# Performance work log

Measured on AMD Instinct MI355X. Metric: run time of the kernel, lower is better.

Reference implementation:

```python
import jax, jax.numpy as jnp
import numpy as np

EPS_POS = 1e-6  # eps passed explicitly for positive cosine_similarity
EPS_NEG = 1e-8  # torch default eps for negative cosine_similarity


def setup_inputs() -> dict:
    key = jax.random.key(0)
    dvectors = jax.random.normal(key, (1024, 32, 256), dtype=jnp.float32)
    w = jnp.array([10.0], dtype=jnp.float32)
    b = jnp.array([-5.0], dtype=jnp.float32)
    return {"dvectors": dvectors, "w": w, "b": b}


def reference(dvectors, w, b):
    S, U, D = dvectors.shape

    # ---- positive: leave-one-out centroid within each speaker ----
    # pos_centroid[s,u] = mean of speaker s's utterances excluding u
    pos_cent = (dvectors.sum(axis=1, keepdims=True) - dvectors) / (U - 1)  # [S,U,D]
    dn_pos = dvectors / jnp.maximum(
        jnp.linalg.norm(dvectors, axis=-1, keepdims=True), EPS_POS)
    cn_pos = pos_cent / jnp.maximum(
        jnp.linalg.norm(pos_cent, axis=-1, keepdims=True), EPS_POS)
    pos_cos = jnp.sum(dn_pos * cn_pos, axis=-1)  # [S,U]

    # ---- negative: full (non-LOO) centroids of every speaker ----
    cent = dvectors.mean(axis=1)  # [S,D]
    dn = dvectors / jnp.maximum(
        jnp.linalg.norm(dvectors, axis=-1, keepdims=True), EPS_NEG)
    cn = cent / jnp.maximum(jnp.linalg.norm(cent, axis=-1, keepdims=True), EPS_NEG)
    all_cos = jnp.einsum('sud,td->sut', dn, cn)  # [S,U,S] cos(dvec[s,u], cent[t])

    # own-speaker entries all_cos[s,u,s] are EXCLUDED from neg_sim
    own = jnp.take_along_axis(
        all_cos, jnp.arange(S, dtype=jnp.int32)[:, None, None], axis=2
    ).squeeze(2)  # [S,U]

    pos_mean = jnp.mean(pos_cos)
    neg_mean = (jnp.sum(all_cos) - jnp.sum(own)) / (S * U * (S - 1))

    # scaled sims: w * cos + b  (torch.clamp(self.w, 1e-6) in forward is a no-op)
    w0 = w[0]
    b0 = b[0]
    pos_scaled = w0 * pos_cos + b0  # [S,U]
    neg_scaled = w0 * all_cos + b0  # [S,U,S]

    # logsumexp over the S-1 other speakers (mask own speaker to -inf)
    own_mask = jnp.eye(S, dtype=bool)[:, None, :]  # [S,1,S]
    neg_masked = jnp.where(own_mask, -jnp.inf, neg_scaled)
    lse = jax.nn.logsumexp(neg_masked, axis=2)  # [S,U]

    loss = jnp.mean(-pos_scaled + lse)
    return (loss, pos_mean, neg_mean)
```

## Files before the change

kernel.cpp:

```cpp
#include <hip/hip_runtime.h>
#include <math.h>

#define NS 1024
#define NU 32
#define ND 256
#define NROWS (NS * NU)
#define BM 128
#define NBLK (NROWS / BM)

static constexpr float EPS_POS = 1e-6f;
static constexpr float EPS_NEG = 1e-8f;

typedef __attribute__((ext_vector_type(8))) short bf16x8;
typedef __attribute__((ext_vector_type(4))) float f32x4;

#if __has_builtin(__builtin_amdgcn_exp2f)
#define EXP2F(x) __builtin_amdgcn_exp2f(x)
#else
#define EXP2F(x) exp2f(x)
#endif

static __device__ __forceinline__ unsigned short f2bf(float f) {
    union { float f; unsigned u; } v; v.f = f;
    unsigned r = v.u + 0x7fffu + ((v.u >> 16) & 1u);
    return (unsigned short)(r >> 16);
}

__global__ __launch_bounds__(256) void ge2e_k1(
    const float* __restrict__ dv, unsigned short* __restrict__ cnb,
    float* __restrict__ invn, float* __restrict__ blk_pos)
{
    const int s = blockIdx.x;
    const int tid = threadIdx.x;
    const int wave = tid >> 6;
    const int lane = tid & 63;

    __shared__ float v[NU][ND];
    __shared__ float cs[ND];
    __shared__ float red[16];

    const float* base = dv + (size_t)s * (NU * ND);
    for (int idx = tid; idx < NU * ND; idx += 256) {
        v[idx >> 8][idx & 255] = base[idx];
    }
    __syncthreads();

    {
        float a = 0.f;
        #pragma unroll
        for (int u = 0; u < NU; ++u) a += v[u][tid];
        cs[tid] = a;
    }
    __syncthreads();

    float c = cs[tid] * (1.0f / NU);
    float p = c * c;
    #pragma unroll
    for (int off = 32; off > 0; off >>= 1) p += __shfl_xor(p, off, 64);
    if (lane == 0) red[wave] = p;
    __syncthreads();
    if (tid == 0) red[8] = red[0] + red[1] + red[2] + red[3];
    __syncthreads();
    {
        float rn = 1.0f / fmaxf(sqrtf(red[8]), EPS_NEG);
        cnb[(size_t)s * ND + tid] = f2bf(c * rn);
    }

    const float inv31 = 1.0f / (NU - 1);
    float pos_part = 0.f;
    const float4 cc = *(const float4*)&cs[lane * 4];
    for (int uu = 0; uu < 8; ++uu) {
        const int u = wave * 8 + uu;
        const float4 vv = *(const float4*)&v[u][lane * 4];
        float pv = 0.f, pp = 0.f, px = 0.f;
        float pc;
        pc = (cc.x - vv.x) * inv31; pv += vv.x * vv.x; pp += pc * pc; px += vv.x * pc;
        pc = (cc.y - vv.y) * inv31; pv += vv.y * vv.y; pp += pc * pc; px += vv.y * pc;
        pc = (cc.z - vv.z) * inv31; pv += vv.z * vv.z; pp += pc * pc; px += vv.z * pc;
        pc = (cc.w - vv.w) * inv31; pv += vv.w * vv.w; pp += pc * pc; px += vv.w * pc;
        #pragma unroll
        for (int off = 32; off > 0; off >>= 1) {
            pv += __shfl_xor(pv, off, 64);
            pp += __shfl_xor(pp, off, 64);
            px += __shfl_xor(px, off, 64);
        }
        if (lane == 0) {
            float nv = sqrtf(pv), npc = sqrtf(pp);
            pos_part += px / (fmaxf(nv, EPS_POS) * fmaxf(npc, EPS_POS));
            invn[s * NU + u] = 1.0f / fmaxf(nv, EPS_NEG);
        }
    }
    if (lane == 0) red[4 + wave] = pos_part;
    __syncthreads();
    if (tid == 0) blk_pos[s] = red[4] + red[5] + red[6] + red[7];
}

__global__ __launch_bounds__(512, 2) void ge2e_k2(
    const float* __restrict__ dv, const unsigned short* __restrict__ cnb,
    const float* __restrict__ invn, const float* __restrict__ wp,
    const float* __restrict__ bp, float* __restrict__ blk_neg,
    float* __restrict__ blk_lse)
{
    const int blk = blockIdx.x;
    const int r0 = blk * BM;
    const int tid = threadIdx.x;
    const int w  = tid >> 6;
    const int l  = tid & 63;
    const int lr = l & 15;
    const int lg = l >> 4;
    const int mg = w >> 2;
    const int ng = w & 3;
    const int rsw = lr & 7;

    __shared__ unsigned short Al[BM][264];
    __shared__ unsigned short Bst[2][64][256];
    __shared__ float sinv[BM];
    __shared__ float pse[4][BM];
    __shared__ float psm[4][BM];
    __shared__ float redn[2], redl[2];

    const float w0 = wp[0];
    const float b0 = bp[0];
    const float c2 = w0 * 1.4426950408889634f;

    if (tid < BM) sinv[tid] = invn[r0 + tid];

    unsigned srcb[4], ldso[4];
    #pragma unroll
    for (int i = 0; i < 4; ++i) {
        const int gi = w * 256 + i * 64 + l;
        const int rr = gi >> 5;
        const int gc = gi & 31;
        srcb[i] = (unsigned)(rr * 512 + (gc ^ (rr & 7)) * 16);
        ldso[i] = (unsigned)(w * 256 + i * 64) * 16;
    }
    const char* cnbc = (const char*)cnb;

    #pragma unroll
    for (int i = 0; i < 4; ++i) {
        __builtin_amdgcn_global_load_lds(
            (const __attribute__((address_space(1))) void*)(cnbc + srcb[i]),
            (__attribute__((address_space(3))) void*)((char*)&Bst[0][0][0] + ldso[i]),
            16, 0, 0);
    }
    __syncthreads();

    #pragma unroll
    for (int it = 0; it < 8; ++it) {
        const int i = tid + it * 512;
        const int row = i >> 5, g = i & 31;
        const float* src = dv + (size_t)(r0 + row) * ND + g * 8;
        const float4 x = *(const float4*)src;
        const float4 y = *(const float4*)(src + 4);
        const float sc = sinv[row];
        uint4 pk;
        pk.x = (unsigned)f2bf(x.x * sc) | ((unsigned)f2bf(x.y * sc) << 16);
        pk.y = (unsigned)f2bf(x.z * sc) | ((unsigned)f2bf(x.w * sc) << 16);
        pk.z = (unsigned)f2bf(y.x * sc) | ((unsigned)f2bf(y.y * sc) << 16);
        pk.w = (unsigned)f2bf(y.z * sc) | ((unsigned)f2bf(y.w * sc) << 16);
        *(uint4*)&Al[row][g * 8] = pk;
    }
    __syncthreads();

    bf16x8 afr[4][8];
    #pragma unroll
    for (int mt = 0; mt < 4; ++mt)
        #pragma unroll
        for (int kt = 0; kt < 8; ++kt)
            afr[mt][kt] = *(const bf16x8*)&Al[mg * 64 + mt * 16 + lr][kt * 32 + lg * 8];
    #pragma unroll
    for (int mt = 0; mt < 4; ++mt)
        #pragma unroll
        for (int kt = 0; kt < 8; ++kt)
            asm volatile("" : "+v"(afr[mt][kt]));

    float se[4][4], sm[4][4];
    #pragma unroll
    for (int mt = 0; mt < 4; ++mt)
        #pragma unroll
        for (int r = 0; r < 4; ++r) { se[mt][r] = 0.f; sm[mt][r] = 0.f; }

    int town[4];
    #pragma unroll
    for (int mt = 0; mt < 4; ++mt) town[mt] = (r0 + mg * 64 + mt * 16) >> 5;

    for (int j = 0; j < 16; ++j) {
        __syncthreads();

        if (j < 15) {
            char* bdst = (char*)&Bst[(j + 1) & 1][0][0];
            const size_t soff = (size_t)(j + 1) * 32768;
            #pragma unroll
            for (int i = 0; i < 4; ++i) {
                __builtin_amdgcn_global_load_lds(
                    (const __attribute__((address_space(1))) void*)(cnbc + soff + srcb[i]),
                    (__attribute__((address_space(3))) void*)(bdst + ldso[i]),
                    16, 0, 0);
            }
        }

        const unsigned short (*bc)[256] = Bst[j & 1];
        f32x4 acc[4];
        #pragma unroll
        for (int mt = 0; mt < 4; ++mt) acc[mt] = (f32x4){0.f, 0.f, 0.f, 0.f};

        #pragma unroll
        for (int kt = 0; kt < 8; ++kt) {
            const bf16x8 bfr = *(const bf16x8*)&bc[ng * 16 + lr][((kt * 4 + lg) ^ rsw) * 8];
            #pragma unroll
            for (int mt = 0; mt < 4; ++mt)
                acc[mt] = __builtin_amdgcn_mfma_f32_16x16x32_bf16(afr[mt][kt], bfr, acc[mt], 0, 0, 0);
        }

        #pragma unroll
        for (int mt = 0; mt < 4; ++mt)
            #pragma unroll
            for (int r = 0; r < 4; ++r) {
                const float cv = acc[mt][r];
                se[mt][r] += EXP2F(fmaf(c2, cv, -c2));
                sm[mt][r] += cv;
            }

        #pragma unroll
        for (int mt = 0; mt < 4; ++mt) {
            const int tn = town[mt];
            if ((tn >> 6) == j && ((tn >> 4) & 3) == ng) {
                if (lr == (tn & 15)) {
                    #pragma unroll
                    for (int r = 0; r < 4; ++r) {
                        const float cv = acc[mt][r];
                        se[mt][r] -= EXP2F(fmaf(c2, cv, -c2));
                        sm[mt][r] -= cv;
                    }
                }
            }
        }
    }

    #pragma unroll
    for (int mask = 1; mask <= 8; mask <<= 1)
        #pragma unroll
        for (int mt = 0; mt < 4; ++mt)
            #pragma unroll
            for (int r = 0; r < 4; ++r) {
                se[mt][r] += __shfl_xor(se[mt][r], mask, 64);
                sm[mt][r] += __shfl_xor(sm[mt][r], mask, 64);
            }

    if (lr == 0) {
        #pragma unroll
        for (int mt = 0; mt < 4; ++mt)
            #pragma unroll
            for (int r = 0; r < 4; ++r) {
                const int row = mg * 64 + mt * 16 + lg * 4 + r;
                pse[ng][row] = se[mt][r];
                psm[ng][row] = sm[mt][r];
            }
    }
    __syncthreads();

    if (tid < BM) {
        const float st = pse[0][tid] + pse[1][tid] + pse[2][tid] + pse[3][tid];
        float smt = psm[0][tid] + psm[1][tid] + psm[2][tid] + psm[3][tid];
        float lse = w0 + b0 + __logf(st);
        #pragma unroll
        for (int mask = 1; mask <= 32; mask <<= 1) {
            lse += __shfl_xor(lse, mask, 64);
            smt += __shfl_xor(smt, mask, 64);
        }
        if ((tid & 63) == 0) { redn[tid >> 6] = smt; redl[tid >> 6] = lse; }
    }
    __syncthreads();
    if (tid == 0) {
        blk_neg[blk] = redn[0] + redn[1];
        blk_lse[blk] = redl[0] + redl[1];
    }
}

__global__ __launch_bounds__(256) void ge2e_k3(
    const float* __restrict__ blk_pos, const float* __restrict__ blk_neg,
    const float* __restrict__ blk_lse, const float* __restrict__ wp,
    const float* __restrict__ bp, float* __restrict__ out)
{
    const int tid = threadIdx.x;
    __shared__ float red[12];
    float p = 0.f, n = 0.f, l = 0.f;
    for (int i = tid; i < NS; i += 256) p += blk_pos[i];
    if (tid < NBLK) { n = blk_neg[tid]; l = blk_lse[tid]; }
    #pragma unroll
    for (int off = 32; off > 0; off >>= 1) {
        p += __shfl_xor(p, off, 64);
        n += __shfl_xor(n, off, 64);
        l += __shfl_xor(l, off, 64);
    }
    const int wave = tid >> 6, lane = tid & 63;
    if (lane == 0) { red[wave] = p; red[4 + wave] = n; red[8 + wave] = l; }
    __syncthreads();
    if (tid == 0) {
        const float ps = red[0] + red[1] + red[2] + red[3];
        const float ns = red[4] + red[5] + red[6] + red[7];
        const float ls = red[8] + red[9] + red[10] + red[11];
        const float pos_mean = ps * (1.0f / NROWS);
        const float neg_mean = ns / ((float)NS * (float)NU * (float)(NS - 1));
        const float lse_mean = ls * (1.0f / NROWS);
        const float loss = -(wp[0] * pos_mean + bp[0]) + lse_mean;
        out[0] = loss;
        out[1] = pos_mean;
        out[2] = neg_mean;
    }
}

extern "C" void kernel_launch(void* const* d_in, const int* in_sizes, int n_in,
                              void* d_out, int out_size, void* d_ws, size_t ws_size,
                              hipStream_t stream)
{
    const float* dv = (const float*)d_in[0];
    const float* w  = (const float*)d_in[1];
    const float* b  = (const float*)d_in[2];
    float* out = (float*)d_out;

    unsigned short* cnb = (unsigned short*)d_ws;
    float* invn    = (float*)(cnb + (size_t)NS * ND);
    float* blk_pos = invn + NROWS;
    float* blk_neg = blk_pos + NS;
    float* blk_lse = blk_neg + NBLK;

    hipLaunchKernelGGL(ge2e_k1, dim3(NS), dim3(256), 0, stream,
                       dv, cnb, invn, blk_pos);
    hipLaunchKernelGGL(ge2e_k2, dim3(NBLK), dim3(512), 0, stream,
                       dv, cnb, invn, w, b, blk_neg, blk_lse);
    hipLaunchKernelGGL(ge2e_k3, dim3(1), dim3(256), 0, stream,
                       blk_pos, blk_neg, blk_lse, w, b, out);
}
```

Before: 53.34 us.

## Precompute normalized bf16 rows in k1 and shrink k2 B tiles

The first kernel now normalizes each utterance row and writes it out as bf16, so the GEMM kernel no longer rereads the fp32 input and converts it through shared memory. The second kernel loads A fragments straight from global memory and splits each block's waves 4x2 instead of 2x4. B tiles drop to 32 centroids per step with twice as many steps, which lowers LDS use and allows launch bounds of 4 blocks per SM. This adds a 16 MB bf16 write in k1 and a 16 MB read in k2, replacing a 32 MB fp32 read, and doubles the number of B-tile syncs.

```diff
diff --git a/kernel.cpp b/kernel.cpp
--- a/kernel.cpp
+++ b/kernel.cpp
@@ -28,7 +28,7 @@
 
 __global__ __launch_bounds__(256) void ge2e_k1(
     const float* __restrict__ dv, unsigned short* __restrict__ cnb,
-    float* __restrict__ invn, float* __restrict__ blk_pos)
+    unsigned short* __restrict__ dnb, float* __restrict__ blk_pos)
 {
     const int s = blockIdx.x;
     const int tid = threadIdx.x;
@@ -37,6 +37,7 @@
 
     __shared__ float v[NU][ND];
     __shared__ float cs[ND];
+    __shared__ float sinvs[NU];
     __shared__ float red[16];
 
     const float* base = dv + (size_t)s * (NU * ND);
@@ -87,19 +88,31 @@
         if (lane == 0) {
             float nv = sqrtf(pv), npc = sqrtf(pp);
             pos_part += px / (fmaxf(nv, EPS_POS) * fmaxf(npc, EPS_POS));
-            invn[s * NU + u] = 1.0f / fmaxf(nv, EPS_NEG);
+            sinvs[u] = 1.0f / fmaxf(nv, EPS_NEG);
         }
     }
     if (lane == 0) red[4 + wave] = pos_part;
     __syncthreads();
     if (tid == 0) blk_pos[s] = red[4] + red[5] + red[6] + red[7];
-}
-
-__global__ __launch_bounds__(512, 2) void ge2e_k2(
-    const float* __restrict__ dv, const unsigned short* __restrict__ cnb,
-    const float* __restrict__ invn, const float* __restrict__ wp,
-    const float* __restrict__ bp, float* __restrict__ blk_neg,
-    float* __restrict__ blk_lse)
+
+    #pragma unroll
+    for (int it = 0; it < 4; ++it) {
+        const int idx = it * 2048 + tid * 8;
+        const int u = idx >> 8, d0 = idx & 255;
+        const float sc = sinvs[u];
+        uint4 pk;
+        pk.x = (unsigned)f2bf(v[u][d0 + 0] * sc) | ((unsigned)f2bf(v[u][d0 + 1] * sc) << 16);
+        pk.y = (unsigned)f2bf(v[u][d0 + 2] * sc) | ((unsigned)f2bf(v[u][d0 + 3] * sc) << 16);
+        pk.z = (unsigned)f2bf(v[u][d0 + 4] * sc) | ((unsigned)f2bf(v[u][d0 + 5] * sc) << 16);
+        pk.w = (unsigned)f2bf(v[u][d0 + 6] * sc) | ((unsigned)f2bf(v[u][d0 + 7] * sc) << 16);
+        *(uint4*)&dnb[(size_t)s * (NU * ND) + idx] = pk;
+    }
+}
+
+__global__ __launch_bounds__(512, 4) void ge2e_k2(
+    const unsigned short* __restrict__ dnb, const unsigned short* __restrict__ cnb,
+    const float* __restrict__ wp, const float* __restrict__ bp,
+    float* __restrict__ blk_neg, float* __restrict__ blk_lse)
 {
     const int blk = blockIdx.x;
     const int r0 = blk * BM;
@@ -108,90 +121,69 @@
     const int l  = tid & 63;
     const int lr = l & 15;
     const int lg = l >> 4;
-    const int mg = w >> 2;
-    const int ng = w & 3;
+    const int mg = w >> 1;
+    const int ng = w & 1;
     const int rsw = lr & 7;
 
-    __shared__ unsigned short Al[BM][264];
-    __shared__ unsigned short Bst[2][64][256];
-    __shared__ float sinv[BM];
-    __shared__ float pse[4][BM];
-    __shared__ float psm[4][BM];
+    __shared__ unsigned short Bst[2][32][256];
+    __shared__ float pse[2][BM];
+    __shared__ float psm[2][BM];
     __shared__ float redn[2], redl[2];
 
     const float w0 = wp[0];
     const float b0 = bp[0];
     const float c2 = w0 * 1.4426950408889634f;
 
-    if (tid < BM) sinv[tid] = invn[r0 + tid];
-
-    unsigned srcb[4], ldso[4];
-    #pragma unroll
-    for (int i = 0; i < 4; ++i) {
-        const int gi = w * 256 + i * 64 + l;
+    unsigned srcb[2], ldso[2];
+    #pragma unroll
+    for (int i = 0; i < 2; ++i) {
+        const int gi = w * 128 + i * 64 + l;
         const int rr = gi >> 5;
         const int gc = gi & 31;
         srcb[i] = (unsigned)(rr * 512 + (gc ^ (rr & 7)) * 16);
-        ldso[i] = (unsigned)(w * 256 + i * 64) * 16;
+        ldso[i] = (unsigned)(w * 128 + i * 64) * 16;
     }
     const char* cnbc = (const char*)cnb;
 
     #pragma unroll
-    for (int i = 0; i < 4; ++i) {
+    for (int i = 0; i < 2; ++i) {
         __builtin_amdgcn_global_load_lds(
             (const __attribute__((address_space(1))) void*)(cnbc + srcb[i]),
             (__attribute__((address_space(3))) void*)((char*)&Bst[0][0][0] + ldso[i]),
             16, 0, 0);
     }
-    __syncthreads();
-
-    #pragma unroll
-    for (int it = 0; it < 8; ++it) {
-        const int i = tid + it * 512;
-        const int row = i >> 5, g = i & 31;
-        const float* src = dv + (size_t)(r0 + row) * ND + g * 8;
-        const float4 x = *(const float4*)src;
-        const float4 y = *(const float4*)(src + 4);
-        const float sc = sinv[row];
-        uint4 pk;
-        pk.x = (unsigned)f2bf(x.x * sc) | ((unsigned)f2bf(x.y * sc) << 16);
-        pk.y = (unsigned)f2bf(x.z * sc) | ((unsigned)f2bf(x.w * sc) << 16);
-        pk.z = (unsigned)f2bf(y.x * sc) | ((unsigned)f2bf(y.y * sc) << 16);
-        pk.w = (unsigned)f2bf(y.z * sc) | ((unsigned)f2bf(y.w * sc) << 16);
-        *(uint4*)&Al[row][g * 8] = pk;
-    }
-    __syncthreads();
-
-    bf16x8 afr[4][8];
-    #pragma unroll
-    for (int mt = 0; mt < 4; ++mt)
+
+    bf16x8 afr[2][8];
+    #pragma unroll
+    for (int mt = 0; mt < 2; ++mt) {
+        const unsigned short* rb = dnb + (size_t)(r0 + mg * 32 + mt * 16 + lr) * ND + lg * 8;
         #pragma unroll
         for (int kt = 0; kt < 8; ++kt)
-            afr[mt][kt] = *(const bf16x8*)&Al[mg * 64 + mt * 16 + lr][kt * 32 + lg * 8];
-    #pragma unroll
-    for (int mt = 0; mt < 4; ++mt)
+            afr[mt][kt] = *(const bf16x8*)(rb + kt * 32);
+    }
+    #pragma unroll
+    for (int mt = 0; mt < 2; ++mt)
         #pragma unroll
         for (int kt = 0; kt < 8; ++kt)
             asm volatile("" : "+v"(afr[mt][kt]));
 
-    float se[4][4], sm[4][4];
-    #pragma unroll
-    for (int mt = 0; mt < 4; ++mt)
+    float se[2][4], sm[2][4];
+    #pragma unroll
+    for (int mt = 0; mt < 2; ++mt)
         #pragma unroll
         for (int r = 0; r < 4; ++r) { se[mt][r] = 0.f; sm[mt][r] = 0.f; }
 
-    int town[4];
-    #pragma unroll
-    for (int mt = 0; mt < 4; ++mt) town[mt] = (r0 + mg * 64 + mt * 16) >> 5;
-
-    for (int j = 0; j < 16; ++j) {
+    const int town = blk * 4 + mg;
+    const int jown = town >> 5, ngown = (town >> 4) & 1, lrown = town & 15;
+
+    for (int j = 0; j < 32; ++j) {
         __syncthreads();
 
-        if (j < 15) {
+        if (j < 31) {
             char* bdst = (char*)&Bst[(j + 1) & 1][0][0];
-            const size_t soff = (size_t)(j + 1) * 32768;
+            const size_t soff = (size_t)(j + 1) * 16384;
             #pragma unroll
-            for (int i = 0; i < 4; ++i) {
+            for (int i = 0; i < 2; ++i) {
                 __builtin_amdgcn_global_load_lds(
                     (const __attribute__((address_space(1))) void*)(cnbc + soff + srcb[i]),
                     (__attribute__((address_space(3))) void*)(bdst + ldso[i]),
@@ -200,38 +192,36 @@
         }
 
         const unsigned short (*bc)[256] = Bst[j & 1];
-        f32x4 acc[4];
-        #pragma unroll
-        for (int mt = 0; mt < 4; ++mt) acc[mt] = (f32x4){0.f, 0.f, 0.f, 0.f};
+        f32x4 acc0 = {0.f, 0.f, 0.f, 0.f};
+        f32x4 acc1 = {0.f, 0.f, 0.f, 0.f};
 
         #pragma unroll
         for (int kt = 0; kt < 8; ++kt) {
             const bf16x8 bfr = *(const bf16x8*)&bc[ng * 16 + lr][((kt * 4 + lg) ^ rsw) * 8];
-            #pragma unroll
-            for (int mt = 0; mt < 4; ++mt)
-                acc[mt] = __builtin_amdgcn_mfma_f32_16x16x32_bf16(afr[mt][kt], bfr, acc[mt], 0, 0, 0);
-        }
-
-        #pragma unroll
-        for (int mt = 0; mt < 4; ++mt)
-            #pragma unroll
-            for (int r = 0; r < 4; ++r) {
-                const float cv = acc[mt][r];
-                se[mt][r] += EXP2F(fmaf(c2, cv, -c2));
-                sm[mt][r] += cv;
-            }
-
-        #pragma unroll
-        for (int mt = 0; mt < 4; ++mt) {
-            const int tn = town[mt];
-            if ((tn >> 6) == j && ((tn >> 4) & 3) == ng) {
-                if (lr == (tn & 15)) {
-                    #pragma unroll
-                    for (int r = 0; r < 4; ++r) {
-                        const float cv = acc[mt][r];
-                        se[mt][r] -= EXP2F(fmaf(c2, cv, -c2));
-                        sm[mt][r] -= cv;
-                    }
+            acc0 = __builtin_amdgcn_mfma_f32_16x16x32_bf16(afr[0][kt], bfr, acc0, 0, 0, 0);
+            acc1 = __builtin_amdgcn_mfma_f32_16x16x32_bf16(afr[1][kt], bfr, acc1, 0, 0, 0);
+        }
+
+        #pragma unroll
+        for (int r = 0; r < 4; ++r) {
+            const float c0_ = acc0[r];
+            se[0][r] += EXP2F(fmaf(c2, c0_, -c2));
+            sm[0][r] += c0_;
+            const float c1_ = acc1[r];
+            se[1][r] += EXP2F(fmaf(c2, c1_, -c2));
+            sm[1][r] += c1_;
+        }
+
+        if (j == jown && ng == ngown) {
+            if (lr == lrown) {
+                #pragma unroll
+                for (int r = 0; r < 4; ++r) {
+                    const float c0_ = acc0[r];
+                    se[0][r] -= EXP2F(fmaf(c2, c0_, -c2));
+                    sm[0][r] -= c0_;
+                    const float c1_ = acc1[r];
+                    se[1][r] -= EXP2F(fmaf(c2, c1_, -c2));
+                    sm[1][r] -= c1_;
                 }
             }
         }
@@ -240,7 +230,7 @@
     #pragma unroll
     for (int mask = 1; mask <= 8; mask <<= 1)
         #pragma unroll
-        for (int mt = 0; mt < 4; ++mt)
+        for (int mt = 0; mt < 2; ++mt)
             #pragma unroll
             for (int r = 0; r < 4; ++r) {
                 se[mt][r] += __shfl_xor(se[mt][r], mask, 64);
@@ -249,10 +239,10 @@
 
     if (lr == 0) {
         #pragma unroll
-        for (int mt = 0; mt < 4; ++mt)
+        for (int mt = 0; mt < 2; ++mt)
             #pragma unroll
             for (int r = 0; r < 4; ++r) {
-                const int row = mg * 64 + mt * 16 + lg * 4 + r;
+                const int row = mg * 32 + mt * 16 + lg * 4 + r;
                 pse[ng][row] = se[mt][r];
                 psm[ng][row] = sm[mt][r];
             }
@@ -260,8 +250,8 @@
     __syncthreads();
 
     if (tid < BM) {
-        const float st = pse[0][tid] + pse[1][tid] + pse[2][tid] + pse[3][tid];
-        float smt = psm[0][tid] + psm[1][tid] + psm[2][tid] + psm[3][tid];
+        const float st = pse[0][tid] + pse[1][tid];
+        float smt = psm[0][tid] + psm[1][tid];
         float lse = w0 + b0 + __logf(st);
         #pragma unroll
         for (int mask = 1; mask <= 32; mask <<= 1) {
@@ -320,15 +310,15 @@
     float* out = (float*)d_out;
 
     unsigned short* cnb = (unsigned short*)d_ws;
-    float* invn    = (float*)(cnb + (size_t)NS * ND);
-    float* blk_pos = invn + NROWS;
+    unsigned short* dnb = cnb + (size_t)NS * ND;
+    float* blk_pos = (float*)(dnb + (size_t)NROWS * ND);
     float* blk_neg = blk_pos + NS;
     float* blk_lse = blk_neg + NBLK;
 
     hipLaunchKernelGGL(ge2e_k1, dim3(NS), dim3(256), 0, stream,
-                       dv, cnb, invn, blk_pos);
+                       dv, cnb, dnb, blk_pos);
     hipLaunchKernelGGL(ge2e_k2, dim3(NBLK), dim3(512), 0, stream,
-                       dv, cnb, invn, w, b, blk_neg, blk_lse);
+                       dnb, cnb, w, b, blk_neg, blk_lse);
     hipLaunchKernelGGL(ge2e_k3, dim3(1), dim3(256), 0, stream,
                        blk_pos, blk_neg, blk_lse, w, b, out);
 }
```

After: 58.35 us. 1.09x slower.

## Precompute normalized bf16 d-vectors in first kernel and shrink GEMM tile

Applied to the files above, without the earlier changes.

The first kernel now writes each row's L2-normalized dvectors as bf16 into a workspace buffer, replacing the per-row inverse-norm array. The similarity kernel loads A fragments directly from that buffer into registers, dropping the fp32 reload, conversion and LDS staging. The row tile is halved to 64 with 256 threads, which doubles the block count and makes every block stream the full centroid matrix. This trades an extra bf16 write and read of the activations for less conversion work and more parallelism, at the cost of twice as much centroid traffic.

```diff
diff --git a/kernel.cpp b/kernel.cpp
--- a/kernel.cpp
+++ b/kernel.cpp
@@ -5,7 +5,7 @@
 #define NU 32
 #define ND 256
 #define NROWS (NS * NU)
-#define BM 128
+#define BM 64
 #define NBLK (NROWS / BM)
 
 static constexpr float EPS_POS = 1e-6f;
@@ -28,7 +28,7 @@
 
 __global__ __launch_bounds__(256) void ge2e_k1(
     const float* __restrict__ dv, unsigned short* __restrict__ cnb,
-    float* __restrict__ invn, float* __restrict__ blk_pos)
+    unsigned short* __restrict__ dnb, float* __restrict__ blk_pos)
 {
     const int s = blockIdx.x;
     const int tid = threadIdx.x;
@@ -37,6 +37,7 @@
 
     __shared__ float v[NU][ND];
     __shared__ float cs[ND];
+    __shared__ float sinvs[NU];
     __shared__ float red[16];
 
     const float* base = dv + (size_t)s * (NU * ND);
@@ -87,87 +88,77 @@
         if (lane == 0) {
             float nv = sqrtf(pv), npc = sqrtf(pp);
             pos_part += px / (fmaxf(nv, EPS_POS) * fmaxf(npc, EPS_POS));
-            invn[s * NU + u] = 1.0f / fmaxf(nv, EPS_NEG);
+            sinvs[u] = 1.0f / fmaxf(nv, EPS_NEG);
         }
     }
     if (lane == 0) red[4 + wave] = pos_part;
     __syncthreads();
     if (tid == 0) blk_pos[s] = red[4] + red[5] + red[6] + red[7];
-}
-
-__global__ __launch_bounds__(512, 2) void ge2e_k2(
-    const float* __restrict__ dv, const unsigned short* __restrict__ cnb,
-    const float* __restrict__ invn, const float* __restrict__ wp,
-    const float* __restrict__ bp, float* __restrict__ blk_neg,
-    float* __restrict__ blk_lse)
+
+    #pragma unroll
+    for (int it = 0; it < 4; ++it) {
+        const int idx = it * 2048 + tid * 8;
+        const int u = idx >> 8, d0 = idx & 255;
+        const float sc = sinvs[u];
+        uint4 pk;
+        pk.x = (unsigned)f2bf(v[u][d0 + 0] * sc) | ((unsigned)f2bf(v[u][d0 + 1] * sc) << 16);
+        pk.y = (unsigned)f2bf(v[u][d0 + 2] * sc) | ((unsigned)f2bf(v[u][d0 + 3] * sc) << 16);
+        pk.z = (unsigned)f2bf(v[u][d0 + 4] * sc) | ((unsigned)f2bf(v[u][d0 + 5] * sc) << 16);
+        pk.w = (unsigned)f2bf(v[u][d0 + 6] * sc) | ((unsigned)f2bf(v[u][d0 + 7] * sc) << 16);
+        *(uint4*)&dnb[(size_t)s * (NU * ND) + idx] = pk;
+    }
+}
+
+__global__ __launch_bounds__(256, 2) void ge2e_k2(
+    const unsigned short* __restrict__ dnb, const unsigned short* __restrict__ cnb,
+    const float* __restrict__ wp, const float* __restrict__ bp,
+    float* __restrict__ blk_neg, float* __restrict__ blk_lse)
 {
     const int blk = blockIdx.x;
     const int r0 = blk * BM;
     const int tid = threadIdx.x;
-    const int w  = tid >> 6;
+    const int ng = tid >> 6;
     const int l  = tid & 63;
     const int lr = l & 15;
     const int lg = l >> 4;
-    const int mg = w >> 2;
-    const int ng = w & 3;
     const int rsw = lr & 7;
 
-    __shared__ unsigned short Al[BM][264];
     __shared__ unsigned short Bst[2][64][256];
-    __shared__ float sinv[BM];
     __shared__ float pse[4][BM];
     __shared__ float psm[4][BM];
-    __shared__ float redn[2], redl[2];
+    __shared__ float redn[1], redl[1];
 
     const float w0 = wp[0];
     const float b0 = bp[0];
     const float c2 = w0 * 1.4426950408889634f;
 
-    if (tid < BM) sinv[tid] = invn[r0 + tid];
-
-    unsigned srcb[4], ldso[4];
-    #pragma unroll
-    for (int i = 0; i < 4; ++i) {
-        const int gi = w * 256 + i * 64 + l;
+    unsigned srcb[8], ldso[8];
+    #pragma unroll
+    for (int i = 0; i < 8; ++i) {
+        const int gi = i * 256 + tid;
         const int rr = gi >> 5;
         const int gc = gi & 31;
         srcb[i] = (unsigned)(rr * 512 + (gc ^ (rr & 7)) * 16);
-        ldso[i] = (unsigned)(w * 256 + i * 64) * 16;
+        ldso[i] = (unsigned)(i * 256 + ng * 64) * 16;
     }
     const char* cnbc = (const char*)cnb;
 
     #pragma unroll
-    for (int i = 0; i < 4; ++i) {
+    for (int i = 0; i < 8; ++i) {
         __builtin_amdgcn_global_load_lds(
             (const __attribute__((address_space(1))) void*)(cnbc + srcb[i]),
             (__attribute__((address_space(3))) void*)((char*)&Bst[0][0][0] + ldso[i]),
             16, 0, 0);
     }
-    __syncthreads();
-
-    #pragma unroll
-    for (int it = 0; it < 8; ++it) {
-        const int i = tid + it * 512;
-        const int row = i >> 5, g = i & 31;
-        const float* src = dv + (size_t)(r0 + row) * ND + g * 8;
-        const float4 x = *(const float4*)src;
-        const float4 y = *(const float4*)(src + 4);
-        const float sc = sinv[row];
-        uint4 pk;
-        pk.x = (unsigned)f2bf(x.x * sc) | ((unsigned)f2bf(x.y * sc) << 16);
-        pk.y = (unsigned)f2bf(x.z * sc) | ((unsigned)f2bf(x.w * sc) << 16);
-        pk.z = (unsigned)f2bf(y.x * sc) | ((unsigned)f2bf(y.y * sc) << 16);
-        pk.w = (unsigned)f2bf(y.z * sc) | ((unsigned)f2bf(y.w * sc) << 16);
-        *(uint4*)&Al[row][g * 8] = pk;
-    }
-    __syncthreads();
 
     bf16x8 afr[4][8];
     #pragma unroll
-    for (int mt = 0; mt < 4; ++mt)
+    for (int mt = 0; mt < 4; ++mt) {
+        const unsigned short* rb = dnb + (size_t)(r0 + mt * 16 + lr) * ND + lg * 8;
         #pragma unroll
         for (int kt = 0; kt < 8; ++kt)
-            afr[mt][kt] = *(const bf16x8*)&Al[mg * 64 + mt * 16 + lr][kt * 32 + lg * 8];
+            afr[mt][kt] = *(const bf16x8*)(rb + kt * 32);
+    }
     #pragma unroll
     for (int mt = 0; mt < 4; ++mt)
         #pragma unroll
@@ -182,7 +173,7 @@
 
     int town[4];
     #pragma unroll
-    for (int mt = 0; mt < 4; ++mt) town[mt] = (r0 + mg * 64 + mt * 16) >> 5;
+    for (int mt = 0; mt < 4; ++mt) town[mt] = blk * 2 + (mt >> 1);
 
     for (int j = 0; j < 16; ++j) {
         __syncthreads();
@@ -191,7 +182,7 @@
             char* bdst = (char*)&Bst[(j + 1) & 1][0][0];
             const size_t soff = (size_t)(j + 1) * 32768;
             #pragma unroll
-            for (int i = 0; i < 4; ++i) {
+            for (int i = 0; i < 8; ++i) {
                 __builtin_amdgcn_global_load_lds(
                     (const __attribute__((address_space(1))) void*)(cnbc + soff + srcb[i]),
                     (__attribute__((address_space(3))) void*)(bdst + ldso[i]),
@@ -252,7 +243,7 @@
         for (int mt = 0; mt < 4; ++mt)
             #pragma unroll
             for (int r = 0; r < 4; ++r) {
-                const int row = mg * 64 + mt * 16 + lg * 4 + r;
+                const int row = mt * 16 + lg * 4 + r;
                 pse[ng][row] = se[mt][r];
                 psm[ng][row] = sm[mt][r];
             }
@@ -268,12 +259,12 @@
             lse += __shfl_xor(lse, mask, 64);
             smt += __shfl_xor(smt, mask, 64);
         }
-        if ((tid & 63) == 0) { redn[tid >> 6] = smt; redl[tid >> 6] = lse; }
+        if (tid == 0) { redn[0] = smt; redl[0] = lse; }
     }
     __syncthreads();
     if (tid == 0) {
-        blk_neg[blk] = redn[0] + redn[1];
-        blk_lse[blk] = redl[0] + redl[1];
+        blk_neg[blk] = redn[0];
+        blk_lse[blk] = redl[0];
     }
 }
 
@@ -286,7 +277,7 @@
     __shared__ float red[12];
     float p = 0.f, n = 0.f, l = 0.f;
     for (int i = tid; i < NS; i += 256) p += blk_pos[i];
-    if (tid < NBLK) { n = blk_neg[tid]; l = blk_lse[tid]; }
+    for (int i = tid; i < NBLK; i += 256) { n += blk_neg[i]; l += blk_lse[i]; }
     #pragma unroll
     for (int off = 32; off > 0; off >>= 1) {
         p += __shfl_xor(p, off, 64);
@@ -320,15 +311,15 @@
     float* out = (float*)d_out;
 
     unsigned short* cnb = (unsigned short*)d_ws;
-    float* invn    = (float*)(cnb + (size_t)NS * ND);
-    float* blk_pos = invn + NROWS;
+    unsigned short* dnb = cnb + (size_t)NS * ND;
+    float* blk_pos = (float*)(dnb + (size_t)NROWS * ND);
     float* blk_neg = blk_pos + NS;
     float* blk_lse = blk_neg + NBLK;
 
     hipLaunchKernelGGL(ge2e_k1, dim3(NS), dim3(256), 0, stream,
-                       dv, cnb, invn, blk_pos);
-    hipLaunchKernelGGL(ge2e_k2, dim3(NBLK), dim3(512), 0, stream,
-                       dv, cnb, invn, w, b, blk_neg, blk_lse);
+                       dv, cnb, dnb, blk_pos);
+    hipLaunchKernelGGL(ge2e_k2, dim3(NBLK), dim3(256), 0, stream,
+                       dnb, cnb, w, b, blk_neg, blk_lse);
     hipLaunchKernelGGL(ge2e_k3, dim3(1), dim3(256), 0, stream,
                        blk_pos, blk_neg, blk_lse, w, b, out);
 }
```

New measurement: 54.73 us. 1.03x slower.
